# Kernel tuning notes

Measured on AMD Instinct MI355X. Metric: run time of the kernel, lower is better.

## Reference

```python
import jax, jax.numpy as jnp
import numpy as np

D_MODEL = 1024
N_HEADS = 16
D_HEAD = D_MODEL // N_HEADS


def setup_inputs() -> dict:
    key = jax.random.key(0)
    kx, kq, kk, kv, ko = jax.random.split(key, 5)
    s = 1.0 / np.sqrt(D_MODEL)  # ~ nn.Linear init scale
    return {
        "x": jax.random.normal(kx, (2, 2048, D_MODEL), dtype=jnp.float32),
        "Wq": jax.random.uniform(kq, (D_MODEL, D_MODEL), jnp.float32, -s, s),
        "Wk": jax.random.uniform(kk, (D_MODEL, D_MODEL), jnp.float32, -s, s),
        "Wv": jax.random.uniform(kv, (D_MODEL, D_MODEL), jnp.float32, -s, s),
        "Wo": jax.random.uniform(ko, (D_MODEL, D_MODEL), jnp.float32, -s, s),
    }


def reference(x, Wq, Wk, Wv, Wo):
    B, T, D = x.shape
    H, Dh = N_HEADS, D_HEAD
    # nn.Linear computes x @ W.T; project then split heads -> [B,H,T,Dh]
    q = (x @ Wq.T).reshape(B, T, H, Dh).transpose(0, 2, 1, 3)
    k = (x @ Wk.T).reshape(B, T, H, Dh).transpose(0, 2, 1, 3)
    v = (x @ Wv.T).reshape(B, T, H, Dh).transpose(0, 2, 1, 3)
    att = jnp.einsum("bhqd,bhkd->bhqk", q, k) / jnp.sqrt(jnp.float32(Dh))
    causal = jnp.tril(jnp.ones((T, T), dtype=bool))  # True = keep
    att = jnp.where(causal[None, None], att, -jnp.inf)
    w = jax.nn.softmax(att, axis=-1)
    out = jnp.einsum("bhqk,bhkd->bhqd", w, v)
    out = out.transpose(0, 2, 1, 3).reshape(B, T, D)
    return out @ Wo.T
```

## Files before the change

kernel.cpp:

```cpp
#include <hip/hip_runtime.h>
#include <hip/hip_bf16.h>

typedef __bf16 bf16;
typedef __bf16 bf16x4 __attribute__((ext_vector_type(4)));
typedef __bf16 bf16x8 __attribute__((ext_vector_type(8)));
typedef float  f32x4  __attribute__((ext_vector_type(4)));

#define DEV static __device__ __forceinline__

DEV void gload_lds16(const void* g, void* l) {
  __builtin_amdgcn_global_load_lds((const __attribute__((address_space(1))) void*)g,
                                   (__attribute__((address_space(3))) void*)l, 16, 0, 0);
}

DEV f32x4 mfma16(bf16x8 a, bf16x8 b, f32x4 c) {
  return __builtin_amdgcn_mfma_f32_16x16x32_bf16(a, b, c, 0, 0, 0);
}

__global__ void convert_all(const float* __restrict__ x,
                            const float* __restrict__ wq, const float* __restrict__ wk,
                            const float* __restrict__ wv, const float* __restrict__ wo,
                            bf16* __restrict__ xb,
                            bf16* __restrict__ wqb, bf16* __restrict__ wkb,
                            bf16* __restrict__ wvb, bf16* __restrict__ wob) {
  const int NX = 4194304;
  const int NW = 1048576;
  const int total4 = (NX + 4 * NW) / 4;
  for (int i = blockIdx.x * blockDim.x + threadIdx.x; i < total4;
       i += gridDim.x * blockDim.x) {
    int e = i * 4;
    const float* src; bf16* dst; int off;
    if (e < NX) { src = x; dst = xb; off = e; }
    else {
      int r = e - NX; int w = r >> 20; off = r & (NW - 1);
      src = (w == 0) ? wq : (w == 1) ? wk : (w == 2) ? wv : wo;
      dst = (w == 0) ? wqb : (w == 1) ? wkb : (w == 2) ? wvb : wob;
    }
    float4 v = *(const float4*)(src + off);
    bf16x4 o; o[0] = (bf16)v.x; o[1] = (bf16)v.y; o[2] = (bf16)v.z; o[3] = (bf16)v.w;
    *(bf16x4*)(dst + off) = o;
  }
}

DEV void stage_tile64(const bf16* gsrc, int grow0, int gcol0, int ld_elems,
                      bf16* lds, int chunk, int l) {
  const int p = chunk * 1024 + l * 16;
  const int r = p >> 7;
  const int cb = (p & 127) ^ ((r & 7) << 4);
  gload_lds16((const char*)gsrc + ((size_t)(grow0 + r) * ld_elems + gcol0) * 2 + cb,
              (char*)lds + p);
}

__global__ __launch_bounds__(256) void gemm_qkv(const bf16* __restrict__ xb,
                                                const bf16* __restrict__ Wq_,
                                                const bf16* __restrict__ Wk_,
                                                const bf16* __restrict__ Wv_,
                                                bf16* __restrict__ Qg,
                                                bf16* __restrict__ Kg,
                                                bf16* __restrict__ Vtg) {
  const int z = blockIdx.z;
  const bf16* A  = (z == 2) ? Wv_ : xb;
  const bf16* Bw = (z == 0) ? Wq_ : (z == 1) ? Wk_ : xb;
  const int K = 1024;
  __shared__ bf16 As[128 * 64];
  __shared__ bf16 Bs[128 * 64];
  const int tid = threadIdx.x, w = tid >> 6, l = tid & 63;
  const int row0 = (z == 2 ? blockIdx.y : blockIdx.x) * 128;
  const int col0 = (z == 2 ? blockIdx.x : blockIdx.y) * 128;
  const int wr = (w >> 1) * 64, wc = (w & 1) * 64;
  const int lr = l & 15, lg = l >> 4;
  const int cxor = lr & 7;
  f32x4 acc[4][4] = {};

  for (int kt = 0; kt < 16; ++kt) {
    const int k0 = kt * 64;
#pragma unroll
    for (int i = 0; i < 4; ++i) {
      const int chunk = w * 4 + i;
      stage_tile64(A,  row0, k0, K, As, chunk, l);
      stage_tile64(Bw, col0, k0, K, Bs, chunk, l);
    }
    __syncthreads();
    bf16x8 af[4][2], bfr[4][2];
#pragma unroll
    for (int m = 0; m < 4; ++m) {
      const int r = wr + m * 16 + lr;
#pragma unroll
      for (int h = 0; h < 2; ++h)
        af[m][h] = *(const bf16x8*)((char*)As + r * 128 + (((h * 4 + lg) ^ cxor) << 4));
    }
#pragma unroll
    for (int n = 0; n < 4; ++n) {
      const int r = wc + n * 16 + lr;
#pragma unroll
      for (int h = 0; h < 2; ++h)
        bfr[n][h] = *(const bf16x8*)((char*)Bs + r * 128 + (((h * 4 + lg) ^ cxor) << 4));
    }
#pragma unroll
    for (int m = 0; m < 4; ++m)
#pragma unroll
      for (int n = 0; n < 4; ++n) {
        acc[m][n] = mfma16(af[m][0], bfr[n][0], acc[m][n]);
        acc[m][n] = mfma16(af[m][1], bfr[n][1], acc[m][n]);
      }
    __syncthreads();
  }

  if (z == 2) {
#pragma unroll
    for (int m = 0; m < 4; ++m)
#pragma unroll
      for (int n = 0; n < 4; ++n)
#pragma unroll
        for (int e = 0; e < 4; ++e) {
          const int rr = row0 + wr + m * 16 + lg * 4 + e;
          const int cc = col0 + wc + n * 16 + lr;
          const int h = rr >> 6, dh = rr & 63;
          const int b = cc >> 11, t = cc & 2047;
          Vtg[(((size_t)(b * 16 + h) * 64) + dh) * 2048 + t] = (bf16)acc[m][n][e];
        }
  } else {
    const float scl = (z == 0) ? 0.18033688011112042f : 1.0f;
    bf16* out = (z == 0) ? Qg : Kg;
#pragma unroll
    for (int m = 0; m < 4; ++m)
#pragma unroll
      for (int n = 0; n < 4; ++n)
#pragma unroll
        for (int e = 0; e < 4; ++e) {
          const int r = row0 + wr + m * 16 + lg * 4 + e;
          const int c = col0 + wc + n * 16 + lr;
          const int b = r >> 11, t = r & 2047;
          const int h = c >> 6,  dh = c & 63;
          out[(((size_t)(b * 16 + h) * 2048) + t) * 64 + dh] = (bf16)(acc[m][n][e] * scl);
        }
  }
}

__global__ __launch_bounds__(256) void attn(const bf16* __restrict__ Qg,
                                            const bf16* __restrict__ Kg,
                                            const bf16* __restrict__ Vtg,
                                            bf16* __restrict__ Obt) {
  const int id  = blockIdx.y * 16 + blockIdx.x;
  const int swz = (id & 7) * 64 + (id >> 3);
  const int bh  = swz >> 4;
  const int x   = swz & 15;
  const int tid = threadIdx.x, w = tid >> 6, l = tid & 63;
  const int lr = l & 15, lg = l >> 4;
  __shared__ bf16 Ks[2][2][4096];
  __shared__ bf16 Vs[2][2][4096];
  __shared__ bf16 Ps[4][1024];
  const size_t base = (size_t)bh * 2048 * 64;
  const char* kbase = (const char*)(Kg + base);
  const char* vbase = (const char*)(Vtg + base);

  const int rA0 = x * 64 + w * 16;
  const int rB0 = (31 - x) * 64 + w * 16;

  bf16x8 qA[2], qB[2];
  {
    const bf16* qp = Qg + base + (size_t)(rA0 + lr) * 64;
    qA[0] = *(const bf16x8*)(qp + lg * 8);
    qA[1] = *(const bf16x8*)(qp + 32 + lg * 8);
    const bf16* qq = Qg + base + (size_t)(rB0 + lr) * 64;
    qB[0] = *(const bf16x8*)(qq + lg * 8);
    qB[1] = *(const bf16x8*)(qq + 32 + lg * 8);
  }
  f32x4 oA[4] = {}, oB[4] = {};
  f32x4 lA = {}, lB = {};

  bf16x8 ones;
#pragma unroll
  for (int j = 0; j < 8; ++j) ones[j] = (bf16)1.0f;

  const int cxor = lr & 7;

  auto stage = [&](int kt, int buf) {
#pragma unroll
    for (int sub = 0; sub < 2; ++sub) {
      const int key0 = kt * 128 + sub * 64;
#pragma unroll
      for (int i = 0; i < 2; ++i) {
        const int p = (w * 2 + i) * 1024 + l * 16;
        const int sw = p ^ (((p >> 7) & 7) << 4);
        gload_lds16(kbase + (size_t)key0 * 128 + sw, (char*)Ks[buf][sub] + p);
        const int vrow = p >> 7;
        const int vcol = (p & 127) ^ (((p >> 7) & 7) << 4);
        gload_lds16(vbase + (size_t)vrow * 4096 + key0 * 2 + vcol,
                    (char*)Vs[buf][sub] + p);
      }
    }
  };

  auto computeTile = [&](int k0, const bf16* Kt, const bf16* Vt, int myrow0,
                         bf16x8 (&qf)[2], f32x4 (&acco)[4], f32x4& lacc) {
    const bool full = (k0 + 63 <= myrow0);
    f32x4 accs[4] = {};
    __builtin_amdgcn_s_setprio(1);
#pragma unroll
    for (int n = 0; n < 4; ++n) {
      const int r = n * 16 + lr;
      bf16x8 kf0 = *(const bf16x8*)((const char*)Kt + r * 128 + ((lg ^ cxor) << 4));
      bf16x8 kf1 = *(const bf16x8*)((const char*)Kt + r * 128 + (((4 + lg) ^ cxor) << 4));
      accs[n] = mfma16(kf0, qf[0], accs[n]);
      accs[n] = mfma16(kf1, qf[1], accs[n]);
    }
    __builtin_amdgcn_s_setprio(0);
    if (!full) {
      const int q = myrow0 + lr;
#pragma unroll
      for (int n = 0; n < 4; ++n) {
        const int keyb = k0 + n * 16 + lg * 4;
#pragma unroll
        for (int e = 0; e < 4; ++e)
          if (keyb + e > q) accs[n][e] = -__builtin_inff();
      }
    }
#pragma unroll
    for (int n = 0; n < 4; ++n)
#pragma unroll
      for (int e = 0; e < 4; ++e) accs[n][e] = exp2f(accs[n][e]);
#pragma unroll
    for (int n = 0; n < 4; ++n) {
      bf16x4 p4;
#pragma unroll
      for (int e = 0; e < 4; ++e) p4[e] = (bf16)accs[n][e];
      const int off = (lr * 128 + (n * 16 + lg * 4) * 2) ^ ((lr & 7) << 4);
      *(bf16x4*)((char*)Ps[w] + off) = p4;
    }
    __builtin_amdgcn_s_setprio(1);
#pragma unroll
    for (int c = 0; c < 2; ++c) {
      bf16x8 pf = *(const bf16x8*)((char*)Ps[w] +
                    (lr * 128 + (((c * 4 + lg) ^ cxor) << 4)));
      lacc = mfma16(pf, ones, lacc);
#pragma unroll
      for (int n = 0; n < 4; ++n) {
        const int r = n * 16 + lr;
        bf16x8 vf = *(const bf16x8*)((const char*)Vt +
                      (r * 128 + (((c * 4 + lg) ^ cxor) << 4)));
        acco[n] = mfma16(pf, vf, acco[n]);
      }
    }
    __builtin_amdgcn_s_setprio(0);
  };

  const int nkt = ((31 - x) >> 1) + 1;
  stage(0, 0);
  int cur = 0;
  for (int kt = 0; kt < nkt; ++kt) {
    __syncthreads();
    if (kt + 1 < nkt) stage(kt + 1, cur ^ 1);
#pragma unroll
    for (int sub = 0; sub < 2; ++sub) {
      const int kk = 2 * kt + sub;
      const int k0 = kk * 64;
      if (kk <= x)
        computeTile(k0, Ks[cur][sub], Vs[cur][sub], rA0, qA, oA, lA);
      if (kk <= 31 - x)
        computeTile(k0, Ks[cur][sub], Vs[cur][sub], rB0, qB, oB, lB);
    }
    cur ^= 1;
  }

  const int b = bh >> 4, h = bh & 15;
  f32x4 invA, invB;
#pragma unroll
  for (int e = 0; e < 4; ++e) {
    invA[e] = __builtin_amdgcn_rcpf(lA[e]);
    invB[e] = __builtin_amdgcn_rcpf(lB[e]);
  }
#pragma unroll
  for (int n = 0; n < 4; ++n)
#pragma unroll
    for (int e = 0; e < 4; ++e) {
      const int rA = rA0 + lg * 4 + e;
      Obt[((size_t)(b * 2048 + rA)) * 1024 + h * 64 + n * 16 + lr] = (bf16)(oA[n][e] * invA[e]);
      const int rB = rB0 + lg * 4 + e;
      Obt[((size_t)(b * 2048 + rB)) * 1024 + h * 64 + n * 16 + lr] = (bf16)(oB[n][e] * invB[e]);
    }
}

__global__ __launch_bounds__(256) void gemm_out(const bf16* __restrict__ A,
                                                const bf16* __restrict__ Bw,
                                                float* __restrict__ Cout) {
  const int K = 1024;
  __shared__ bf16 As[128 * 64];
  __shared__ bf16 Bs[64 * 64];
  const int tid = threadIdx.x, w = tid >> 6, l = tid & 63;
  const int row0 = blockIdx.x * 128, col0 = blockIdx.y * 64;
  const int wr = (w >> 1) * 64, wc = (w & 1) * 32;
  const int lr = l & 15, lg = l >> 4;
  const int cxor = lr & 7;
  f32x4 acc[4][2] = {};

  for (int kt = 0; kt < 16; ++kt) {
    const int k0 = kt * 64;
#pragma unroll
    for (int i = 0; i < 4; ++i)
      stage_tile64(A, row0, k0, K, As, w * 4 + i, l);
#pragma unroll
    for (int i = 0; i < 2; ++i)
      stage_tile64(Bw, col0, k0, K, Bs, w * 2 + i, l);
    __syncthreads();
    bf16x8 af[4][2], bfr[2][2];
#pragma unroll
    for (int m = 0; m < 4; ++m) {
      const int r = wr + m * 16 + lr;
#pragma unroll
      for (int h = 0; h < 2; ++h)
        af[m][h] = *(const bf16x8*)((char*)As + r * 128 + (((h * 4 + lg) ^ cxor) << 4));
    }
#pragma unroll
    for (int n = 0; n < 2; ++n) {
      const int r = wc + n * 16 + lr;
#pragma unroll
      for (int h = 0; h < 2; ++h)
        bfr[n][h] = *(const bf16x8*)((char*)Bs + r * 128 + (((h * 4 + lg) ^ cxor) << 4));
    }
#pragma unroll
    for (int m = 0; m < 4; ++m)
#pragma unroll
      for (int n = 0; n < 2; ++n) {
        acc[m][n] = mfma16(af[m][0], bfr[n][0], acc[m][n]);
        acc[m][n] = mfma16(af[m][1], bfr[n][1], acc[m][n]);
      }
    __syncthreads();
  }

#pragma unroll
  for (int m = 0; m < 4; ++m)
#pragma unroll
    for (int n = 0; n < 2; ++n)
#pragma unroll
      for (int e = 0; e < 4; ++e) {
        const int r = row0 + wr + m * 16 + lg * 4 + e;
        const int c = col0 + wc + n * 16 + lr;
        Cout[(size_t)r * 1024 + c] = acc[m][n][e];
      }
}

extern "C" void kernel_launch(void* const* d_in, const int* in_sizes, int n_in,
                              void* d_out, int out_size, void* d_ws, size_t ws_size,
                              hipStream_t stream) {
  const float* x  = (const float*)d_in[0];
  const float* wq = (const float*)d_in[1];
  const float* wk = (const float*)d_in[2];
  const float* wv = (const float*)d_in[3];
  const float* wo = (const float*)d_in[4];
  float* out = (float*)d_out;

  bf16* xb  = (bf16*)d_ws;
  bf16* wqb = xb  + 4194304;
  bf16* wkb = wqb + 1048576;
  bf16* wvb = wkb + 1048576;
  bf16* wob = wvb + 1048576;
  bf16* Qg  = wob + 1048576;
  bf16* Kg  = Qg  + 4194304;
  bf16* Vtg = Kg  + 4194304;
  bf16* Obt = Vtg + 4194304;

  convert_all<<<2048, 256, 0, stream>>>(x, wq, wk, wv, wo, xb, wqb, wkb, wvb, wob);
  gemm_qkv<<<dim3(32, 8, 3), 256, 0, stream>>>(xb, wqb, wkb, wvb, Qg, Kg, Vtg);
  attn<<<dim3(16, 32), 256, 0, stream>>>(Qg, Kg, Vtg, Obt);
  gemm_out<<<dim3(32, 16), 256, 0, stream>>>(Obt, wob, out);
}
```

Before: 106.1 us.

## Split attention key tiles across two wave groups with LDS reduction

Doubles the attention block to 512 threads. Each of two 4-wave groups processes one of the two 64-key subtiles per 128-key stage, instead of one group processing both serially. At the end, the partial output and row-sum accumulators are combined through shared memory before normalisation and store. This raises per-block parallelism and latency hiding on the causal attention loop, at the cost of an extra barrier, an LDS exchange, and more threads per block, which may limit occupancy.

```diff
diff --git a/kernel.cpp b/kernel.cpp
--- a/kernel.cpp
+++ b/kernel.cpp
@@ -137,7 +137,7 @@
   }
 }
 
-__global__ __launch_bounds__(256) void attn(const bf16* __restrict__ Qg,
+__global__ __launch_bounds__(512) void attn(const bf16* __restrict__ Qg,
                                             const bf16* __restrict__ Kg,
                                             const bf16* __restrict__ Vtg,
                                             bf16* __restrict__ Obt) {
@@ -146,16 +146,18 @@
   const int bh  = swz >> 4;
   const int x   = swz & 15;
   const int tid = threadIdx.x, w = tid >> 6, l = tid & 63;
+  const int g = w >> 2, wq = w & 3;
   const int lr = l & 15, lg = l >> 4;
-  __shared__ bf16 Ks[2][2][4096];
-  __shared__ bf16 Vs[2][2][4096];
-  __shared__ bf16 Ps[4][1024];
+  __shared__ char smem[81920];
+  bf16* KsB = (bf16*)smem;
+  bf16* VsB = (bf16*)(smem + 32768);
+  bf16* PsW = (bf16*)(smem + 65536) + w * 1024;
   const size_t base = (size_t)bh * 2048 * 64;
   const char* kbase = (const char*)(Kg + base);
   const char* vbase = (const char*)(Vtg + base);
 
-  const int rA0 = x * 64 + w * 16;
-  const int rB0 = (31 - x) * 64 + w * 16;
+  const int rA0 = x * 64 + wq * 16;
+  const int rB0 = (31 - x) * 64 + wq * 16;
 
   bf16x8 qA[2], qB[2];
   {
@@ -177,18 +179,18 @@
 
   auto stage = [&](int kt, int buf) {
 #pragma unroll
-    for (int sub = 0; sub < 2; ++sub) {
+    for (int i = 0; i < 2; ++i) {
+      const int c = w * 2 + i;
+      const int sub = c >> 3;
       const int key0 = kt * 128 + sub * 64;
-#pragma unroll
-      for (int i = 0; i < 2; ++i) {
-        const int p = (w * 2 + i) * 1024 + l * 16;
-        const int sw = p ^ (((p >> 7) & 7) << 4);
-        gload_lds16(kbase + (size_t)key0 * 128 + sw, (char*)Ks[buf][sub] + p);
-        const int vrow = p >> 7;
-        const int vcol = (p & 127) ^ (((p >> 7) & 7) << 4);
-        gload_lds16(vbase + (size_t)vrow * 4096 + key0 * 2 + vcol,
-                    (char*)Vs[buf][sub] + p);
-      }
+      const int p = (c & 7) * 1024 + l * 16;
+      const int sw = p ^ (((p >> 7) & 7) << 4);
+      gload_lds16(kbase + (size_t)key0 * 128 + sw,
+                  (char*)KsB + (buf * 2 + sub) * 8192 + p);
+      const int vrow = p >> 7;
+      const int vcol = (p & 127) ^ (((p >> 7) & 7) << 4);
+      gload_lds16(vbase + (size_t)vrow * 4096 + key0 * 2 + vcol,
+                  (char*)VsB + (buf * 2 + sub) * 8192 + p);
     }
   };
 
@@ -226,12 +228,12 @@
 #pragma unroll
       for (int e = 0; e < 4; ++e) p4[e] = (bf16)accs[n][e];
       const int off = (lr * 128 + (n * 16 + lg * 4) * 2) ^ ((lr & 7) << 4);
-      *(bf16x4*)((char*)Ps[w] + off) = p4;
+      *(bf16x4*)((char*)PsW + off) = p4;
     }
     __builtin_amdgcn_s_setprio(1);
 #pragma unroll
     for (int c = 0; c < 2; ++c) {
-      bf16x8 pf = *(const bf16x8*)((char*)Ps[w] +
+      bf16x8 pf = *(const bf16x8*)((char*)PsW +
                     (lr * 128 + (((c * 4 + lg) ^ cxor) << 4)));
       lacc = mfma16(pf, ones, lacc);
 #pragma unroll
@@ -251,34 +253,65 @@
   for (int kt = 0; kt < nkt; ++kt) {
     __syncthreads();
     if (kt + 1 < nkt) stage(kt + 1, cur ^ 1);
-#pragma unroll
-    for (int sub = 0; sub < 2; ++sub) {
-      const int kk = 2 * kt + sub;
-      const int k0 = kk * 64;
-      if (kk <= x)
-        computeTile(k0, Ks[cur][sub], Vs[cur][sub], rA0, qA, oA, lA);
-      if (kk <= 31 - x)
-        computeTile(k0, Ks[cur][sub], Vs[cur][sub], rB0, qB, oB, lB);
-    }
+    const int kk = 2 * kt + g;
+    const int k0 = kk * 64;
+    const bf16* Kt = KsB + (cur * 2 + g) * 4096;
+    const bf16* Vt = VsB + (cur * 2 + g) * 4096;
+    if (kk <= x)
+      computeTile(k0, Kt, Vt, rA0, qA, oA, lA);
+    if (kk <= 31 - x)
+      computeTile(k0, Kt, Vt, rB0, qB, oB, lB);
     cur ^= 1;
   }
 
-  const int b = bh >> 4, h = bh & 15;
-  f32x4 invA, invB;
-#pragma unroll
-  for (int e = 0; e < 4; ++e) {
-    invA[e] = __builtin_amdgcn_rcpf(lA[e]);
-    invB[e] = __builtin_amdgcn_rcpf(lB[e]);
-  }
-#pragma unroll
-  for (int n = 0; n < 4; ++n)
+  __syncthreads();
+  float* xch = (float*)smem;
+  const int xbase = (wq * 64 + l) * 41;
+  if (g == 1) {
+#pragma unroll
+    for (int n = 0; n < 4; ++n)
+#pragma unroll
+      for (int e = 0; e < 4; ++e) {
+        xch[xbase + n * 4 + e]      = oA[n][e];
+        xch[xbase + 16 + n * 4 + e] = oB[n][e];
+      }
 #pragma unroll
     for (int e = 0; e < 4; ++e) {
-      const int rA = rA0 + lg * 4 + e;
-      Obt[((size_t)(b * 2048 + rA)) * 1024 + h * 64 + n * 16 + lr] = (bf16)(oA[n][e] * invA[e]);
-      const int rB = rB0 + lg * 4 + e;
-      Obt[((size_t)(b * 2048 + rB)) * 1024 + h * 64 + n * 16 + lr] = (bf16)(oB[n][e] * invB[e]);
-    }
+      xch[xbase + 32 + e] = lA[e];
+      xch[xbase + 36 + e] = lB[e];
+    }
+  }
+  __syncthreads();
+  if (g == 0) {
+#pragma unroll
+    for (int n = 0; n < 4; ++n)
+#pragma unroll
+      for (int e = 0; e < 4; ++e) {
+        oA[n][e] += xch[xbase + n * 4 + e];
+        oB[n][e] += xch[xbase + 16 + n * 4 + e];
+      }
+#pragma unroll
+    for (int e = 0; e < 4; ++e) {
+      lA[e] += xch[xbase + 32 + e];
+      lB[e] += xch[xbase + 36 + e];
+    }
+    const int b = bh >> 4, h = bh & 15;
+    f32x4 invA, invB;
+#pragma unroll
+    for (int e = 0; e < 4; ++e) {
+      invA[e] = __builtin_amdgcn_rcpf(lA[e]);
+      invB[e] = __builtin_amdgcn_rcpf(lB[e]);
+    }
+#pragma unroll
+    for (int n = 0; n < 4; ++n)
+#pragma unroll
+      for (int e = 0; e < 4; ++e) {
+        const int rA = rA0 + lg * 4 + e;
+        Obt[((size_t)(b * 2048 + rA)) * 1024 + h * 64 + n * 16 + lr] = (bf16)(oA[n][e] * invA[e]);
+        const int rB = rB0 + lg * 4 + e;
+        Obt[((size_t)(b * 2048 + rB)) * 1024 + h * 64 + n * 16 + lr] = (bf16)(oB[n][e] * invB[e]);
+      }
+  }
 }
 
 __global__ __launch_bounds__(256) void gemm_out(const bf16* __restrict__ A,
@@ -362,6 +395,6 @@
 
   convert_all<<<2048, 256, 0, stream>>>(x, wq, wk, wv, wo, xb, wqb, wkb, wvb, wob);
   gemm_qkv<<<dim3(32, 8, 3), 256, 0, stream>>>(xb, wqb, wkb, wvb, Qg, Kg, Vtg);
-  attn<<<dim3(16, 32), 256, 0, stream>>>(Qg, Kg, Vtg, Obt);
+  attn<<<dim3(16, 32), 512, 0, stream>>>(Qg, Kg, Vtg, Obt);
   gemm_out<<<dim3(32, 16), 256, 0, stream>>>(Obt, wob, out);
 }
```

New measurement: 96.79 us, median of 2. 8.8% less time.
